# Kernel tuning notes

Measured on AMD Instinct MI355X. Metric: run time of the kernel, lower is better.

Reference implementation:

```python
import jax, jax.numpy as jnp
import numpy as np

N_SIGNALS = 2048
HID = 16  # importance_hidden_dim


def _layernorm(x, g, b, eps=1e-5):
    mu = jnp.mean(x, axis=-1, keepdims=True)
    var = jnp.mean((x - mu) ** 2, axis=-1, keepdims=True)
    return (x - mu) / jnp.sqrt(var + eps) * g + b


def _gelu(x):
    return jax.nn.gelu(x, approximate=False)  # torch nn.GELU default (erf)


def _pairwise_features(p):
    # p: [n, 15] normalized params
    dt = jnp.abs(p[:, None, 5] - p[None, :, 5])
    dra = jnp.abs(p[:, None, 3] - p[None, :, 3])
    ddec = jnp.abs(p[:, None, 4] - p[None, :, 4])
    sky_sep = jnp.sqrt(dra ** 2 + ddec ** 2)
    m1 = p[:, 0] * 95 + 5
    m2 = p[:, 1] * 95 + 5
    mc = (m1 * m2) ** 0.6 / (m1 + m2) ** 0.2  # chirp mass
    mass_sim = 1.0 / (1.0 + jnp.abs(mc[:, None] - mc[None, :]) / 30.0)
    f_isco = 220.0 / (m1 + m2)
    freq_overlap = jnp.exp(-jnp.abs(f_isco[:, None] - f_isco[None, :]) / 100.0)
    dist = p[:, 2] * 2950 + 50
    dist_ratio = jnp.minimum(dist[:, None], dist[None, :]) / jnp.maximum(dist[:, None], dist[None, :])
    dpsi = jnp.abs(p[:, None, 7] - p[None, :, 7])
    # [n, n, 8]
    return jnp.stack([dt, sky_sep, mass_sim, freq_overlap, dist_ratio, dpsi, dra, ddec], axis=-1)


def setup_inputs() -> dict:
    key = jax.random.key(0)
    ks = jax.random.split(key, 16)
    n = N_SIGNALS
    params_batch = jax.random.uniform(ks[0], (n, 15), dtype=jnp.float32)
    def lin(k, out_d, in_d):
        lim = 1.0 / np.sqrt(in_d)
        kw, kb = jax.random.split(k)
        w = jax.random.uniform(kw, (out_d, in_d), minval=-lim, maxval=lim, dtype=jnp.float32)
        b = jax.random.uniform(kb, (out_d,), minval=-lim, maxval=lim, dtype=jnp.float32)
        return w, b
    iw1, ib1 = lin(ks[1], HID, 8)
    iw2, ib2 = lin(ks[2], 1, HID)
    ow1, ob1 = lin(ks[3], 32, 8)
    ow2, ob2 = lin(ks[4], 16, 32)
    return {
        "params_batch": params_batch,
        "iw1": iw1, "ib1": ib1,
        "ig1": jnp.ones((HID,), jnp.float32), "ibt1": jnp.zeros((HID,), jnp.float32),
        "iw2": iw2, "ib2": ib2,
        "ow1": ow1, "ob1": ob1,
        "og1": jnp.ones((32,), jnp.float32), "obt1": jnp.zeros((32,), jnp.float32),
        "ow2": ow2, "ob2": ob2,
    }


def reference(params_batch, iw1, ib1, ig1, ibt1, iw2, ib2, ow1, ob1, og1, obt1, ow2, ob2):
    n = params_batch.shape[0]
    feats = _pairwise_features(params_batch)  # [n, n, 8]
    # importance net (dropout is identity at inference)
    h = _gelu(_layernorm(jnp.einsum('ijf,hf->ijh', feats, iw1) + ib1, ig1, ibt1))
    logits = jnp.einsum('ijh,oh->ijo', h, iw2)[..., 0] + ib2[0]  # [n, n]
    # exclude self-pairs (j == i) from the softmax, matching the i != j loop
    diag = jnp.eye(n, dtype=bool)
    logits = jnp.where(diag, -jnp.inf, logits)
    attn = jax.nn.softmax(logits, axis=1)  # [n, n]
    weighted = jnp.einsum('ij,ijf->if', attn, feats)  # [n, 8]
    # overlap net
    h2 = _gelu(_layernorm(weighted @ ow1.T + ob1, og1, obt1))
    return h2 @ ow2.T + ob2  # [n, 16]
```

## Files before the change

kernel.cpp:

```cpp
#include <hip/hip_runtime.h>

#define N_SIG 2048
#define NT    32
#define N_OFFDIAG_BLOCKS 992
#define N_PAIR_BLOCKS 1024
#define DV_FLOATS   (N_SIG * 8)
#define PART_FLOATS (32 * 64 * 9 * 64)

__device__ __forceinline__ float frcp(float x) { return __builtin_amdgcn_rcpf(x); }

__device__ __forceinline__ float erf_div_sqrt2(float y) {
    const float ay = fabsf(y);
    const float t  = frcp(fmaf(0.23164454f, ay, 1.f));
    const float p  = t * fmaf(t, fmaf(t, fmaf(t, fmaf(t, 1.061405429f, -1.453152027f),
                                              1.421413741f), -0.284496736f), 0.254829592f);
    const float e  = __expf(-0.5f * ay * ay);
    return copysignf(fmaf(-p, e, 1.f), y);
}

template<bool ZERO_ACC>
__global__ void derive_k(const float* __restrict__ p, float* __restrict__ dv,
                         float* __restrict__ acc) {
    int j = blockIdx.x * blockDim.x + threadIdx.x;
    if (j >= N_SIG) return;
    if constexpr (ZERO_ACC) {
        #pragma unroll
        for (int k = 0; k < 9; k++) acc[j * 9 + k] = 0.f;
    }
    const float* pj = p + j * 15;
    float m1 = pj[0] * 95.f + 5.f, m2 = pj[1] * 95.f + 5.f;
    float mc = powf(m1 * m2, 0.6f) / powf(m1 + m2, 0.2f);
    float fisco = 220.f / (m1 + m2);
    float dist = pj[2] * 2950.f + 50.f;
    float4* o = (float4*)(dv + j * 8);
    o[0] = make_float4(pj[5], pj[3], pj[4], mc);
    o[1] = make_float4(fisco, dist, pj[7], 0.f);
}

template<bool USE_PART>
__global__ __launch_bounds__(256) void pair_k(
    const float* __restrict__ dv,
    const float* __restrict__ iw1, const float* __restrict__ ib1,
    const float* __restrict__ ig1, const float* __restrict__ ibt1,
    const float* __restrict__ iw2,
    float* __restrict__ acc)
{
    __shared__ float4 sColA[64], sColB[64];
    __shared__ __align__(16) float sW1[128];
    __shared__ __align__(16) float sEC[64];
    __shared__ float partR[9 * 256];
    __shared__ float partC[USE_PART ? 9 * 256 : 1];

    const int b = blockIdx.x;
    int ti, tj, half;
    bool diag;
    if (b < N_OFFDIAG_BLOCKS) {
        const int tileId = b >> 1;
        half = b & 1;
        int k = tileId, row = 0;
        while (k >= NT - 1 - row) { k -= NT - 1 - row; row++; }
        ti = row; tj = row + 1 + k;
        diag = false;
    } else {
        ti = tj = b - N_OFFDIAG_BLOCKS;
        half = 0;
        diag = true;
    }
    const int rbase = ti * 64, cbase = tj * 64;

    const int tid = threadIdx.x;
    const float4* dv4 = (const float4*)dv;

    if (tid < 64)  { sColA[tid] = dv4[(cbase + tid) * 2]; sColB[tid] = dv4[(cbase + tid) * 2 + 1]; }
    if (tid >= 64 && tid < 192) sW1[tid - 64] = iw1[tid - 64];
    if (tid >= 192 && tid < 208) {
        int h = tid - 192;
        sEC[h * 4 + 0] = ib1[h]; sEC[h * 4 + 1] = ig1[h];
        sEC[h * 4 + 2] = ibt1[h]; sEC[h * 4 + 3] = 0.5f * iw2[h];
    }
    __syncthreads();

    const int w = tid >> 6, l = tid & 63;
    const int gi = rbase + l;
    const float4 r0 = dv4[gi * 2], r1 = dv4[gi * 2 + 1];
    const float ti_ = r0.x, rai = r0.y, deci = r0.z, mci = r0.w;
    const float fi = r1.x, disti = r1.y, psii = r1.z;

    const int sstep = diag ? 4 : 8;
    const int sbase = diag ? (w + 1) : (half * 4 + w);

    float rowacc[9], colacc[9];
    #pragma unroll
    for (int q = 0; q < 9; q++) { rowacc[q] = 0.f; colacc[q] = 0.f; }

    const float4* sW4  = (const float4*)sW1;
    const float4* sEC4 = (const float4*)sEC;

    for (int t = 0; t < 8; t++) {
        const int s  = sbase + sstep * t;
        const int dj = (l + s) & 63;
        const float4 c0 = sColA[dj], c1 = sColB[dj];

        const float dra  = fabsf(rai - c0.y), ddec = fabsf(deci - c0.z);
        float f[8];
        f[0] = fabsf(ti_ - c0.x);
        f[1] = __builtin_amdgcn_sqrtf(fmaf(dra, dra, ddec * ddec));
        f[2] = frcp(fmaf(fabsf(mci - c0.w), 0.033333333f, 1.f));
        f[3] = __expf(fabsf(fi - c1.x) * -0.01f);
        f[4] = fminf(disti, c1.y) * frcp(fmaxf(disti, c1.y));
        f[5] = fabsf(psii - c1.z);
        f[6] = dra; f[7] = ddec;

        float z[16];
        float s1 = 0.f, s2 = 0.f;
        #pragma unroll
        for (int h = 0; h < 16; h++) {
            const float4 w0 = sW4[h * 2];
            const float4 w1 = sW4[h * 2 + 1];
            float zv = sEC4[h].x;
            zv = fmaf(w0.x, f[0], zv); zv = fmaf(w0.y, f[1], zv);
            zv = fmaf(w0.z, f[2], zv); zv = fmaf(w0.w, f[3], zv);
            zv = fmaf(w1.x, f[4], zv); zv = fmaf(w1.y, f[5], zv);
            zv = fmaf(w1.z, f[6], zv); zv = fmaf(w1.w, f[7], zv);
            z[h] = zv;
            s1 += zv; s2 = fmaf(zv, zv, s2);
        }
        const float mu  = s1 * 0.0625f;
        const float var = fmaf(-mu, mu, s2 * 0.0625f);
        const float inv = __builtin_amdgcn_rsqf(var + 1e-5f);

        float logit = 0.f;
        #pragma unroll
        for (int h = 0; h < 16; h++) {
            const float4 c = sEC4[h];
            const float y = fmaf((z[h] - mu) * inv, c.y, c.z);
            logit = fmaf(y * c.w, 1.f + erf_div_sqrt2(y), logit);
        }
        float e = __expf(logit);
        if (diag && s == 32 && l >= 32) e = 0.f;

        rowacc[8] += e; colacc[8] += e;
        #pragma unroll
        for (int q = 0; q < 8; q++) {
            rowacc[q] = fmaf(e, f[q], rowacc[q]);
            colacc[q] = fmaf(e, f[q], colacc[q]);
        }
        if (t + 1 < 8) {
            const int src = (l + sstep) & 63;
            #pragma unroll
            for (int q = 0; q < 9; q++) colacc[q] = __shfl(colacc[q], src);
        }
    }

    const int s_last = sbase + sstep * 7;
    const int cfin = (l + s_last) & 63;

    if constexpr (USE_PART) {
        #pragma unroll
        for (int q = 0; q < 9; q++) partR[q * 256 + w * 64 + l]    = rowacc[q];
        #pragma unroll
        for (int q = 0; q < 9; q++) partC[q * 256 + w * 64 + cfin] = colacc[q];
        __syncthreads();
        if (tid < 192) {
            const int sig = tid & 63;
            float* __restrict__ pr = acc + ((ti * 64 + (2 * tj + half)) * 9) * 64;
            float* __restrict__ pc = acc + ((tj * 64 + (2 * ti + 1 - half)) * 9) * 64;
            #pragma unroll
            for (int r = 0; r < 3; r++) {
                const int q = (tid >> 6) * 3 + r;
                const float* ppR = partR + q * 256 + sig;
                pr[q * 64 + sig] = ppR[0] + ppR[64] + ppR[128] + ppR[192];
                const float* ppC = partC + q * 256 + sig;
                pc[q * 64 + sig] = ppC[0] + ppC[64] + ppC[128] + ppC[192];
            }
        }
    } else {
        const int stag = b & 63;
        #pragma unroll
        for (int q = 0; q < 9; q++) partR[q * 256 + w * 64 + l] = rowacc[q];
        __syncthreads();
        if (tid < 192) {
            const int sig = (tid + stag) & 63;
            #pragma unroll
            for (int r = 0; r < 3; r++) {
                const int q = (tid >> 6) * 3 + r;
                const float* pp = partR + q * 256 + sig;
                unsafeAtomicAdd(&acc[(rbase + sig) * 9 + q], pp[0] + pp[64] + pp[128] + pp[192]);
            }
        }
        __syncthreads();
        #pragma unroll
        for (int q = 0; q < 9; q++) partR[q * 256 + w * 64 + cfin] = colacc[q];
        __syncthreads();
        if (tid < 192) {
            const int sig = (tid + stag) & 63;
            #pragma unroll
            for (int r = 0; r < 3; r++) {
                const int q = (tid >> 6) * 3 + r;
                const float* pp = partR + q * 256 + sig;
                unsafeAtomicAdd(&acc[(cbase + sig) * 9 + q], pp[0] + pp[64] + pp[128] + pp[192]);
            }
        }
    }
}

template<bool USE_PART>
__global__ void out_k(const float* __restrict__ accp,
                      const float* __restrict__ ow1, const float* __restrict__ ob1,
                      const float* __restrict__ og1, const float* __restrict__ obt1,
                      const float* __restrict__ ow2, const float* __restrict__ ob2,
                      float* __restrict__ out)
{
    __shared__ float h2s[32];
    const int t = threadIdx.x;
    int i;
    float a9[9];
    if constexpr (USE_PART) {
        const int b = blockIdx.x;
        i = (b & 7) * 256 + (b >> 3);
        const int g = i >> 6, sig = i & 63;
        #pragma unroll
        for (int q = 0; q < 9; q++) {
            float v = accp[(((g * 64 + t) * 9) + q) * 64 + sig];
            #pragma unroll
            for (int off = 32; off > 0; off >>= 1) v += __shfl_xor(v, off);
            a9[q] = v;
        }
    } else {
        i = blockIdx.x;
        if (t < 32) {
            #pragma unroll
            for (int q = 0; q < 9; q++) a9[q] = accp[i * 9 + q];
        }
    }
    if (t < 32) {
        const float invL = frcp(a9[8]);
        float z2 = ob1[t];
        #pragma unroll
        for (int f = 0; f < 8; f++) z2 = fmaf(ow1[t * 8 + f], a9[f] * invL, z2);
        float mu = z2;
        #pragma unroll
        for (int off = 16; off > 0; off >>= 1) mu += __shfl_xor(mu, off);
        mu *= (1.f / 32.f);
        const float d = z2 - mu;
        float var = d * d;
        #pragma unroll
        for (int off = 16; off > 0; off >>= 1) var += __shfl_xor(var, off);
        var *= (1.f / 32.f);
        const float y = d * __builtin_amdgcn_rsqf(var + 1e-5f) * og1[t] + obt1[t];
        h2s[t] = 0.5f * y * (1.f + erf_div_sqrt2(y));
    }
    __syncthreads();
    if (t < 16) {
        float o = ob2[t];
        #pragma unroll
        for (int k = 0; k < 32; k++) o = fmaf(ow2[t * 32 + k], h2s[k], o);
        out[i * 16 + t] = o;
    }
}

extern "C" void kernel_launch(void* const* d_in, const int* in_sizes, int n_in,
                              void* d_out, int out_size, void* d_ws, size_t ws_size,
                              hipStream_t stream) {
    const float* p    = (const float*)d_in[0];
    const float* iw1  = (const float*)d_in[1];
    const float* ib1  = (const float*)d_in[2];
    const float* ig1  = (const float*)d_in[3];
    const float* ibt1 = (const float*)d_in[4];
    const float* iw2  = (const float*)d_in[5];
    const float* ow1  = (const float*)d_in[7];
    const float* ob1  = (const float*)d_in[8];
    const float* og1  = (const float*)d_in[9];
    const float* obt1 = (const float*)d_in[10];
    const float* ow2  = (const float*)d_in[11];
    const float* ob2  = (const float*)d_in[12];

    float* dv = (float*)d_ws;
    const bool use_part = ws_size >= (size_t)(DV_FLOATS + PART_FLOATS) * sizeof(float);

    if (use_part) {
        float* part = dv + DV_FLOATS;
        derive_k<false><<<N_SIG / 256, 256, 0, stream>>>(p, dv, nullptr);
        pair_k<true><<<N_PAIR_BLOCKS, 256, 0, stream>>>(dv, iw1, ib1, ig1, ibt1, iw2, part);
        out_k<true><<<N_SIG, 64, 0, stream>>>(part, ow1, ob1, og1, obt1, ow2, ob2,
                                              (float*)d_out);
    } else {
        float* acc = dv + DV_FLOATS;
        derive_k<true><<<N_SIG / 256, 256, 0, stream>>>(p, dv, acc);
        pair_k<false><<<N_PAIR_BLOCKS, 256, 0, stream>>>(dv, iw1, ib1, ig1, ibt1, iw2, acc);
        out_k<false><<<N_SIG, 64, 0, stream>>>(acc, ow1, ob1, og1, obt1, ow2, ob2,
                                               (float*)d_out);
    }
}
```

Before: 118.6 us.

## Read importance-net weights directly from global memory and restructure final reduction kernel

The pair kernel no longer stages the importance-net weights and LayerNorm constants in shared memory. It reads them straight from global memory with uniform indices, so the compiler can turn them into scalar loads that are shared across the wavefront. The output stage is replaced by a 32-block kernel: each block sums 64 partial slots per group with coalesced loads into shared memory, then runs the overlap MLP for 64 signals, instead of launching 2048 small blocks that each do a strided gather. The new output kernel has far fewer blocks, so parallelism is lower, and it adds a serial 64-slot loop. Any gain depends on the partition layout it reads matching what the pair kernel writes.

```diff
diff --git a/kernel.cpp b/kernel.cpp
--- a/kernel.cpp
+++ b/kernel.cpp
@@ -46,8 +46,6 @@
     float* __restrict__ acc)
 {
     __shared__ float4 sColA[64], sColB[64];
-    __shared__ __align__(16) float sW1[128];
-    __shared__ __align__(16) float sEC[64];
     __shared__ float partR[9 * 256];
     __shared__ float partC[USE_PART ? 9 * 256 : 1];
 
@@ -72,12 +70,6 @@
     const float4* dv4 = (const float4*)dv;
 
     if (tid < 64)  { sColA[tid] = dv4[(cbase + tid) * 2]; sColB[tid] = dv4[(cbase + tid) * 2 + 1]; }
-    if (tid >= 64 && tid < 192) sW1[tid - 64] = iw1[tid - 64];
-    if (tid >= 192 && tid < 208) {
-        int h = tid - 192;
-        sEC[h * 4 + 0] = ib1[h]; sEC[h * 4 + 1] = ig1[h];
-        sEC[h * 4 + 2] = ibt1[h]; sEC[h * 4 + 3] = 0.5f * iw2[h];
-    }
     __syncthreads();
 
     const int w = tid >> 6, l = tid & 63;
@@ -92,9 +84,6 @@
     float rowacc[9], colacc[9];
     #pragma unroll
     for (int q = 0; q < 9; q++) { rowacc[q] = 0.f; colacc[q] = 0.f; }
-
-    const float4* sW4  = (const float4*)sW1;
-    const float4* sEC4 = (const float4*)sEC;
 
     for (int t = 0; t < 8; t++) {
         const int s  = sbase + sstep * t;
@@ -115,13 +104,10 @@
         float s1 = 0.f, s2 = 0.f;
         #pragma unroll
         for (int h = 0; h < 16; h++) {
-            const float4 w0 = sW4[h * 2];
-            const float4 w1 = sW4[h * 2 + 1];
-            float zv = sEC4[h].x;
-            zv = fmaf(w0.x, f[0], zv); zv = fmaf(w0.y, f[1], zv);
-            zv = fmaf(w0.z, f[2], zv); zv = fmaf(w0.w, f[3], zv);
-            zv = fmaf(w1.x, f[4], zv); zv = fmaf(w1.y, f[5], zv);
-            zv = fmaf(w1.z, f[6], zv); zv = fmaf(w1.w, f[7], zv);
+            const float* wrow = iw1 + h * 8;
+            float zv = ib1[h];
+            #pragma unroll
+            for (int q = 0; q < 8; q++) zv = fmaf(wrow[q], f[q], zv);
             z[h] = zv;
             s1 += zv; s2 = fmaf(zv, zv, s2);
         }
@@ -132,9 +118,9 @@
         float logit = 0.f;
         #pragma unroll
         for (int h = 0; h < 16; h++) {
-            const float4 c = sEC4[h];
-            const float y = fmaf((z[h] - mu) * inv, c.y, c.z);
-            logit = fmaf(y * c.w, 1.f + erf_div_sqrt2(y), logit);
+            const float y   = fmaf((z[h] - mu) * inv, ig1[h], ibt1[h]);
+            const float phi = fmaf(0.5f, erf_div_sqrt2(y), 0.5f);
+            logit = fmaf(y * iw2[h], phi, logit);
         }
         float e = __expf(logit);
         if (diag && s == 32 && l >= 32) e = 0.f;
@@ -204,40 +190,86 @@
     }
 }
 
-template<bool USE_PART>
-__global__ void out_k(const float* __restrict__ accp,
+__global__ __launch_bounds__(256) void outfused_k(
+    const float* __restrict__ part,
+    const float* __restrict__ ow1, const float* __restrict__ ob1,
+    const float* __restrict__ og1, const float* __restrict__ obt1,
+    const float* __restrict__ ow2, const float* __restrict__ ob2,
+    float* __restrict__ out)
+{
+    __shared__ float red[576];
+    __shared__ float sOw1[32 * 9];
+    __shared__ float sOw2T[32 * 16];
+    __shared__ float sB1[32], sG[32], sBt[32], sB2[16];
+    __shared__ float h2s[8 * 33];
+
+    const int g = blockIdx.x;
+    const int tid = threadIdx.x;
+
+    { int h = tid >> 3, f = tid & 7; sOw1[h * 9 + f] = ow1[tid]; }
+    { int o = tid >> 5, k = tid & 31; sOw2T[k * 16 + o] = ow2[tid]; }
+    { int idx = tid + 256; int o = idx >> 5, k = idx & 31; sOw2T[k * 16 + o] = ow2[idx]; }
+    if (tid < 32) { sB1[tid] = ob1[tid]; sG[tid] = og1[tid]; sBt[tid] = obt1[tid]; }
+    if (tid < 16) sB2[tid] = ob2[tid];
+
+    const float* bp = part + g * (64 * 576);
+    float a0 = 0.f, a1 = 0.f, a2 = 0.f;
+    #pragma unroll 4
+    for (int slot = 0; slot < 64; ++slot) {
+        const float* ps = bp + slot * 576;
+        a0 += ps[tid];
+        a1 += ps[tid + 256];
+        if (tid < 64) a2 += ps[tid + 512];
+    }
+    red[tid] = a0; red[tid + 256] = a1; if (tid < 64) red[tid + 512] = a2;
+    __syncthreads();
+
+    const int grp = tid >> 5;
+    const int h   = tid & 31;
+
+    for (int pass = 0; pass < 8; ++pass) {
+        const int sig = pass * 8 + grp;
+        const float invL = frcp(red[8 * 64 + sig]);
+        float z2 = sB1[h];
+        #pragma unroll
+        for (int f = 0; f < 8; f++)
+            z2 = fmaf(sOw1[h * 9 + f], red[f * 64 + sig] * invL, z2);
+        float mu = z2;
+        #pragma unroll
+        for (int off = 16; off > 0; off >>= 1) mu += __shfl_xor(mu, off);
+        mu *= (1.f / 32.f);
+        const float d = z2 - mu;
+        float var = d * d;
+        #pragma unroll
+        for (int off = 16; off > 0; off >>= 1) var += __shfl_xor(var, off);
+        var *= (1.f / 32.f);
+        const float y = d * __builtin_amdgcn_rsqf(var + 1e-5f) * sG[h] + sBt[h];
+        h2s[grp * 33 + h] = 0.5f * y * (1.f + erf_div_sqrt2(y));
+        __syncthreads();
+        if (h < 16) {
+            float o = sB2[h];
+            #pragma unroll
+            for (int k = 0; k < 32; k++)
+                o = fmaf(sOw2T[k * 16 + h], h2s[grp * 33 + k], o);
+            out[(g * 64 + sig) * 16 + h] = o;
+        }
+        __syncthreads();
+    }
+}
+
+__global__ void out_k(const float* __restrict__ acc,
                       const float* __restrict__ ow1, const float* __restrict__ ob1,
                       const float* __restrict__ og1, const float* __restrict__ obt1,
                       const float* __restrict__ ow2, const float* __restrict__ ob2,
                       float* __restrict__ out)
 {
     __shared__ float h2s[32];
-    const int t = threadIdx.x;
-    int i;
-    float a9[9];
-    if constexpr (USE_PART) {
-        const int b = blockIdx.x;
-        i = (b & 7) * 256 + (b >> 3);
-        const int g = i >> 6, sig = i & 63;
-        #pragma unroll
-        for (int q = 0; q < 9; q++) {
-            float v = accp[(((g * 64 + t) * 9) + q) * 64 + sig];
-            #pragma unroll
-            for (int off = 32; off > 0; off >>= 1) v += __shfl_xor(v, off);
-            a9[q] = v;
-        }
-    } else {
-        i = blockIdx.x;
-        if (t < 32) {
-            #pragma unroll
-            for (int q = 0; q < 9; q++) a9[q] = accp[i * 9 + q];
-        }
-    }
+    const int i = blockIdx.x, t = threadIdx.x;
     if (t < 32) {
-        const float invL = frcp(a9[8]);
+        const float invL = frcp(acc[i * 9 + 8]);
         float z2 = ob1[t];
         #pragma unroll
-        for (int f = 0; f < 8; f++) z2 = fmaf(ow1[t * 8 + f], a9[f] * invL, z2);
+        for (int f = 0; f < 8; f++) z2 = fmaf(ow1[t * 8 + f], acc[i * 9 + f] * invL, z2);
         float mu = z2;
         #pragma unroll
         for (int off = 16; off > 0; off >>= 1) mu += __shfl_xor(mu, off);
@@ -282,13 +314,13 @@
         float* part = dv + DV_FLOATS;
         derive_k<false><<<N_SIG / 256, 256, 0, stream>>>(p, dv, nullptr);
         pair_k<true><<<N_PAIR_BLOCKS, 256, 0, stream>>>(dv, iw1, ib1, ig1, ibt1, iw2, part);
-        out_k<true><<<N_SIG, 64, 0, stream>>>(part, ow1, ob1, og1, obt1, ow2, ob2,
-                                              (float*)d_out);
+        outfused_k<<<32, 256, 0, stream>>>(part, ow1, ob1, og1, obt1, ow2, ob2,
+                                           (float*)d_out);
     } else {
         float* acc = dv + DV_FLOATS;
         derive_k<true><<<N_SIG / 256, 256, 0, stream>>>(p, dv, acc);
         pair_k<false><<<N_PAIR_BLOCKS, 256, 0, stream>>>(dv, iw1, ib1, ig1, ibt1, iw2, acc);
-        out_k<false><<<N_SIG, 64, 0, stream>>>(acc, ow1, ob1, og1, obt1, ow2, ob2,
-                                               (float*)d_out);
-    }
-}
+        out_k<<<N_SIG, 64, 0, stream>>>(acc, ow1, ob1, og1, obt1, ow2, ob2,
+                                        (float*)d_out);
+    }
+}
```

Result: slower. 154.5 us (+30.2%).
